# Optimization experiments

Hardware: AMD Instinct MI355X
Metric: run time of the kernel (lower is better)

The kernel has to match this reference:

```python
import jax, jax.numpy as jnp
import numpy as np

B, P, Q, N, D = 64, 12, 12, 1024, 64
DOW, TOD = 7, 288  # day-of-week / time-of-day one-hot depths (GMAN STEmbedding)


def setup_inputs() -> dict:
    key = jax.random.key(0)
    ks = iter(jax.random.split(key, 40))
    def g(shape, scale=0.05):
        return jax.random.normal(next(ks), shape, jnp.float32) * scale
    inp = {
        "X": jax.random.normal(next(ks), (B, P, N), jnp.float32),
        "ZC": jax.random.normal(next(ks), (B, P, 400), jnp.float32),
        "ZF": jax.random.normal(next(ks), (B, P, 1600), jnp.float32),
        "SE": g((N, D)),
        # STEmbedding FCs
        "W_se1": g((D, D)), "b_se1": jnp.zeros((D,), jnp.float32),
        "W_se2": g((D, D)), "b_se2": jnp.zeros((D,), jnp.float32),
        "W_te1": g((DOW + TOD, D)), "b_te1": jnp.zeros((D,), jnp.float32),
        "W_te2": g((D, D)), "b_te2": jnp.zeros((D,), jnp.float32),
        # FC_X_in
        "W_in1": g((1, D)), "b_in1": jnp.zeros((D,), jnp.float32),
        "W_in2": g((D, D)), "b_in2": jnp.zeros((D,), jnp.float32),
        # DCGRU layer 1 (gconv over [x||state, support@(x||state)] -> 4D input)
        "Wg1": g((4 * D, 2 * D)), "bg1": jnp.ones((2 * D,), jnp.float32),
        "Wc1": g((4 * D, D)), "bc1": jnp.zeros((D,), jnp.float32),
        # DCGRU layer 2
        "Wg2": g((4 * D, 2 * D)), "bg2": jnp.ones((2 * D,), jnp.float32),
        "Wc2": g((4 * D, D)), "bc2": jnp.zeros((D,), jnp.float32),
        # FC_X_out
        "W_o1": g((D, D)), "b_o1": jnp.zeros((D,), jnp.float32),
        "W_o2": g((D, Q)), "b_o2": jnp.zeros((Q,), jnp.float32),
        "TE": jax.random.randint(next(ks), (B, P + Q, 2), 0, 7, jnp.int32),
    }
    return inp


def _dcgru_scan(x_seq, support, Wg, bg, Wc, bc):
    """x_seq: [B,P,N,D] -> (sequence [B,P,N,D], last state [B,N,D])."""
    def gconv(x, s, W, b):
        z = jnp.concatenate([x, s], -1)                      # [B,N,2D]
        z1 = jnp.einsum('nm,bmd->bnd', support, z)           # diffusion step K=1
        return jnp.concatenate([z, z1], -1) @ W + b

    def step(state, x_t):
        ru = jax.nn.sigmoid(gconv(x_t, state, Wg, bg))       # [B,N,2D]
        r, u = jnp.split(ru, 2, axis=-1)
        c = jnp.tanh(gconv(x_t, r * state, Wc, bc))
        new = u * state + (1.0 - u) * c
        return new, new

    state0 = jnp.zeros(x_seq.shape[:1] + x_seq.shape[2:], x_seq.dtype)
    last, seq = jax.lax.scan(step, state0, jnp.swapaxes(x_seq, 0, 1))
    return jnp.swapaxes(seq, 0, 1), last


def reference(X, ZC, ZF, SE, W_se1, b_se1, W_se2, b_se2, W_te1, b_te1,
              W_te2, b_te2, W_in1, b_in1, W_in2, b_in2,
              Wg1, bg1, Wc1, bc1, Wg2, bg2, Wc2, bc2,
              W_o1, b_o1, W_o2, b_o2, TE):
    # adjacency is identity in this module; random_walk(I).T == I
    adj = jnp.eye(N, dtype=jnp.float32)
    support = (adj / jnp.sum(adj, axis=1, keepdims=True)).T

    # STEmbedding: spatial + temporal embedding
    se = jax.nn.relu(SE @ W_se1 + b_se1) @ W_se2 + b_se2                 # [N,D]
    te_oh = jnp.concatenate([
        jax.nn.one_hot(TE[..., 0], DOW, dtype=jnp.float32),
        jax.nn.one_hot(TE[..., 1], TOD, dtype=jnp.float32)], -1)        # [B,P+Q,295]
    te = jax.nn.relu(te_oh @ W_te1 + b_te1) @ W_te2 + b_te2              # [B,P+Q,D]
    STEX = (se[None, None] + te[:, :, None, :])[:, :P]                   # [B,P,N,D]

    # FC_X_in on expanded X, add STE
    Xe = X[..., None]                                                    # [B,P,N,1]
    Xe = jax.nn.relu(Xe @ W_in1 + b_in1) @ W_in2 + b_in2                 # [B,P,N,D]
    Xe = Xe + STEX

    seq1, _ = _dcgru_scan(Xe, support, Wg1, bg1, Wc1, bc1)               # [B,P,N,D]
    _, h = _dcgru_scan(seq1, support, Wg2, bg2, Wc2, bc2)                # [B,N,D]

    Y = jax.nn.relu(h @ W_o1 + b_o1) @ W_o2 + b_o2                       # [B,N,Q]
    return jnp.transpose(Y, (0, 2, 1))                                   # [B,Q,N]
```

## Files before the change

### kernel.cpp

```cpp
#include <hip/hip_runtime.h>


#define NB 1024

typedef float f32x4 __attribute__((ext_vector_type(4)));
typedef __bf16 bf16x8 __attribute__((ext_vector_type(8)));
typedef int i32x4 __attribute__((ext_vector_type(4)));

#define MFMA(a, b, c) __builtin_amdgcn_mfma_f32_16x16x32_bf16(a, b, c, 0, 0, 0)

__device__ __forceinline__ float fexp(float x) {
    return __builtin_amdgcn_exp2f(x * 1.44269504088896341f);
}
__device__ __forceinline__ float fsigmoid(float x) {
    return __builtin_amdgcn_rcpf(1.0f + fexp(-x));
}
__device__ __forceinline__ float ftanh(float x) {
    return 1.0f - 2.0f * __builtin_amdgcn_rcpf(1.0f + fexp(2.0f * x));
}

__device__ __forceinline__ bf16x8 ldfrag(const unsigned short* p) {
    i32x4 t = *(const i32x4*)p;
    return __builtin_bit_cast(bf16x8, t);
}
__device__ __forceinline__ void split8(f32x4 a0, f32x4 a1, bf16x8& hi, bf16x8& lo) {
    #pragma unroll
    for (int i = 0; i < 4; i++) {
        __bf16 h0 = (__bf16)a0[i]; hi[i] = h0;     lo[i] = (__bf16)(a0[i] - (float)h0);
        __bf16 h1 = (__bf16)a1[i]; hi[4 + i] = h1; lo[4 + i] = (__bf16)(a1[i] - (float)h1);
    }
}
__device__ __forceinline__ void wsplit(float v, unsigned short* dhi, unsigned short* dlo) {
    __bf16 h = (__bf16)v;
    __bf16 l = (__bf16)(v - (float)h);
    *dhi = __builtin_bit_cast(unsigned short, h);
    *dlo = __builtin_bit_cast(unsigned short, l);
}


__global__ void prep_gates(const float* __restrict__ Wg1, const float* __restrict__ Wg2,
                           unsigned short* __restrict__ fr) {
    int i = blockIdx.x * 256 + threadIdx.x;
    if (i >= 4096) return;
    int layer = i >> 11, r = i & 2047;
    int w = r >> 9; r &= 511; int nt = r >> 8; r &= 255; int ks = r >> 6; int lane = r & 63;
    const float* Wg = layer ? Wg2 : Wg1;
    int n = lane & 15, q = lane >> 4;
    int col = nt ? (64 + w * 16 + n) : (w * 16 + n);
    unsigned short* dst = fr + layer * 32768 + (((w * 2 + nt) * 4 + ks) * 2) * 512 + lane * 8;
    #pragma unroll
    for (int j = 0; j < 8; j++) {
        int k = ks * 32 + q * 8 + j;
        float v = Wg[k * 128 + col] + Wg[(k + 128) * 128 + col];
        wsplit(v, dst + j, dst + 512 + j);
    }
}

__global__ void prep_cand(const float* __restrict__ Wc1, const float* __restrict__ Wc2,
                          unsigned short* __restrict__ fr) {
    int i = blockIdx.x * 256 + threadIdx.x;
    if (i >= 2048) return;
    int layer = i >> 10, r = i & 1023;
    int w = r >> 8; r &= 255; int ks = r >> 6; int lane = r & 63;
    const float* Wc = layer ? Wc2 : Wc1;
    int n = lane & 15, q = lane >> 4;
    int col = w * 16 + n;
    unsigned short* dst = fr + 65536 + layer * 16384 + ((w * 4 + ks) * 2) * 512 + lane * 8;
    #pragma unroll
    for (int j = 0; j < 8; j++) {
        int k = ks * 32 + q * 8 + j;
        float v = Wc[k * 64 + col] + Wc[(k + 128) * 64 + col];
        wsplit(v, dst + j, dst + 512 + j);
    }
}

__global__ void prep_small(const float* __restrict__ Win2, const float* __restrict__ Wo1,
                           unsigned short* __restrict__ fr) {
    int i = blockIdx.x * 256 + threadIdx.x;
    if (i >= 1024) return;
    int kind = i >> 9, r = i & 511;
    int w = r >> 7; r &= 127; int ks = r >> 6; int lane = r & 63;
    const float* W = kind ? Wo1 : Win2;
    int n = lane & 15, q = lane >> 4;
    int col = w * 16 + n;
    unsigned short* dst = fr + 98304 + kind * 8192 + ((w * 2 + ks) * 2) * 512 + lane * 8;
    #pragma unroll
    for (int j = 0; j < 8; j++) {
        int k = ks * 32 + q * 8 + j;
        float v = W[k * 64 + col];
        wsplit(v, dst + j, dst + 512 + j);
    }
}

__global__ void prep_se(const float* __restrict__ SE, const float* __restrict__ W1,
                        const float* __restrict__ b1, const float* __restrict__ W2,
                        const float* __restrict__ b2, const float* __restrict__ bin2,
                        float* __restrict__ seB) {
    __shared__ float h[64];
    int n = blockIdx.x, d = threadIdx.x;
    float acc = b1[d];
    for (int k = 0; k < 64; k++) acc = fmaf(SE[n * 64 + k], W1[k * 64 + d], acc);
    h[d] = fmaxf(acc, 0.0f);
    __syncthreads();
    float acc2 = b2[d];
    for (int k = 0; k < 64; k++) acc2 = fmaf(h[k], W2[k * 64 + d], acc2);
    int nb = n >> 6, tok = n & 63;
    int mt = tok >> 4, q = (tok >> 2) & 3, r = tok & 3;
    int w = d >> 4, n16 = d & 15;
    seB[(((nb * 4 + w) * 64) + q * 16 + n16) * 16 + mt * 4 + r] = acc2 + bin2[d];
}

__global__ void prep_te(const int* __restrict__ TE, const float* __restrict__ W1,
                        const float* __restrict__ b1, const float* __restrict__ W2,
                        const float* __restrict__ b2, float* __restrict__ teo) {
    __shared__ float h[64];
    int bp = blockIdx.x;
    int b = bp / 12, p = bp - b * 12;
    int d = threadIdx.x;
    int dow = TE[(b * 24 + p) * 2 + 0];
    int tod = TE[(b * 24 + p) * 2 + 1];
    float v = W1[dow * 64 + d] + W1[(7 + tod) * 64 + d] + b1[d];
    h[d] = fmaxf(v, 0.0f);
    __syncthreads();
    float acc = b2[d];
    for (int k = 0; k < 64; k++) acc = fmaf(h[k], W2[k * 64 + d], acc);
    teo[bp * 64 + d] = acc;
}

#define SW(t, k) ((t) * 64 + ((k) ^ (((t) & 3) << 3) ^ ((t) & 4)))

__device__ __forceinline__ void lda_split(const float* __restrict__ src, int m, int k0,
                                          bf16x8& ahi, bf16x8& alo) {
    const int sk = (k0 ^ ((m & 3) << 3) ^ (m & 4));
    f32x4 a0 = *(const f32x4*)(src + m * 64 + sk);
    f32x4 a1 = *(const f32x4*)(src + m * 64 + (sk ^ 4));
    split8(a0, a1, ahi, alo);
}

__device__ __forceinline__ void gru_layer(
    const float* __restrict__ XIN, float* __restrict__ S, float* __restrict__ RS,
    const unsigned short* __restrict__ frG, const unsigned short* __restrict__ frC,
    const float* __restrict__ bg, const float* __restrict__ bc, int l, int w) {
    const int n16 = l & 15, q = l >> 4;
    const int col = w * 16 + n16;
    f32x4 accR[4], accU[4], accC[4];
    #pragma unroll
    for (int mt = 0; mt < 4; mt++) {
        accR[mt] = (f32x4)0.0f; accU[mt] = (f32x4)0.0f; accC[mt] = (f32x4)0.0f;
    }
    #pragma unroll
    for (int ks = 0; ks < 2; ks++) {
        bf16x8 bhiR = ldfrag(frG + ((0 * 4 + ks) * 2 + 0) * 512 + l * 8);
        bf16x8 bloR = ldfrag(frG + ((0 * 4 + ks) * 2 + 1) * 512 + l * 8);
        bf16x8 bhiU = ldfrag(frG + ((1 * 4 + ks) * 2 + 0) * 512 + l * 8);
        bf16x8 bloU = ldfrag(frG + ((1 * 4 + ks) * 2 + 1) * 512 + l * 8);
        bf16x8 bhiC = ldfrag(frC + (ks * 2 + 0) * 512 + l * 8);
        bf16x8 bloC = ldfrag(frC + (ks * 2 + 1) * 512 + l * 8);
        const int kk = ks * 32 + q * 8;
        #pragma unroll
        for (int mt = 0; mt < 4; mt++) {
            bf16x8 ahi, alo;
            lda_split(XIN, mt * 16 + n16, kk, ahi, alo);
            accR[mt] = MFMA(ahi, bhiR, accR[mt]);
            accR[mt] = MFMA(alo, bhiR, accR[mt]);
            accR[mt] = MFMA(ahi, bloR, accR[mt]);
            accU[mt] = MFMA(ahi, bhiU, accU[mt]);
            accU[mt] = MFMA(alo, bhiU, accU[mt]);
            accU[mt] = MFMA(ahi, bloU, accU[mt]);
            accC[mt] = MFMA(ahi, bhiC, accC[mt]);
            accC[mt] = MFMA(alo, bhiC, accC[mt]);
            accC[mt] = MFMA(ahi, bloC, accC[mt]);
        }
    }
    #pragma unroll
    for (int ks = 2; ks < 4; ks++) {
        bf16x8 bhiR = ldfrag(frG + ((0 * 4 + ks) * 2 + 0) * 512 + l * 8);
        bf16x8 bloR = ldfrag(frG + ((0 * 4 + ks) * 2 + 1) * 512 + l * 8);
        bf16x8 bhiU = ldfrag(frG + ((1 * 4 + ks) * 2 + 0) * 512 + l * 8);
        bf16x8 bloU = ldfrag(frG + ((1 * 4 + ks) * 2 + 1) * 512 + l * 8);
        const int kk = (ks - 2) * 32 + q * 8;
        #pragma unroll
        for (int mt = 0; mt < 4; mt++) {
            bf16x8 ahi, alo;
            lda_split(S, mt * 16 + n16, kk, ahi, alo);
            accR[mt] = MFMA(ahi, bhiR, accR[mt]);
            accR[mt] = MFMA(alo, bhiR, accR[mt]);
            accR[mt] = MFMA(ahi, bloR, accR[mt]);
            accU[mt] = MFMA(ahi, bhiU, accU[mt]);
            accU[mt] = MFMA(alo, bhiU, accU[mt]);
            accU[mt] = MFMA(ahi, bloU, accU[mt]);
        }
    }
    const float bgr = bg[col];
    #pragma unroll
    for (int mt = 0; mt < 4; mt++)
        #pragma unroll
        for (int r = 0; r < 4; r++) {
            int tok = mt * 16 + q * 4 + r;
            RS[SW(tok, col)] = fsigmoid(accR[mt][r] + bgr) * S[SW(tok, col)];
        }
    __syncthreads();
    #pragma unroll
    for (int ks = 2; ks < 4; ks++) {
        bf16x8 bhi = ldfrag(frC + (ks * 2 + 0) * 512 + l * 8);
        bf16x8 blo = ldfrag(frC + (ks * 2 + 1) * 512 + l * 8);
        const int kk = (ks - 2) * 32 + q * 8;
        #pragma unroll
        for (int mt = 0; mt < 4; mt++) {
            bf16x8 ahi, alo;
            lda_split(RS, mt * 16 + n16, kk, ahi, alo);
            accC[mt] = MFMA(ahi, bhi, accC[mt]);
            accC[mt] = MFMA(alo, bhi, accC[mt]);
            accC[mt] = MFMA(ahi, blo, accC[mt]);
        }
    }
    const float bcc = bc[col], bgu = bg[64 + col];
    #pragma unroll
    for (int mt = 0; mt < 4; mt++)
        #pragma unroll
        for (int r = 0; r < 4; r++) {
            int tok = mt * 16 + q * 4 + r;
            float u = fsigmoid(accU[mt][r] + bgu);
            float cnd = ftanh(accC[mt][r] + bcc);
            int a = SW(tok, col);
            S[a] = u * S[a] + (1.0f - u) * cnd;
        }
    __syncthreads();
}

__global__ __launch_bounds__(256, 2) void gman_main(
    const float* __restrict__ X, const float* __restrict__ ws,
    const float* __restrict__ Win1, const float* __restrict__ bin1,
    const float* __restrict__ bg1, const float* __restrict__ bc1,
    const float* __restrict__ bg2, const float* __restrict__ bc2,
    const float* __restrict__ bo1, const float* __restrict__ Wo2,
    const float* __restrict__ bo2, float* __restrict__ out) {
    __shared__ float XE[4096], S1[4096], S2[4096], RS[4096];

    const int tid = threadIdx.x;
    const int l = tid & 63;
    const int w = tid >> 6;
    const int n16 = l & 15, q = l >> 4;
    const int col = w * 16 + n16;
    const int b = blockIdx.x >> 4;
    const int nb = blockIdx.x & 15;
    const int n0 = nb << 6;

    const unsigned short* frU = (const unsigned short*)ws;
    const unsigned short* frG1 = frU + w * 8192;
    const unsigned short* frG2 = frU + 32768 + w * 8192;
    const unsigned short* frC1 = frU + 65536 + w * 4096;
    const unsigned short* frC2 = frU + 81920 + w * 4096;
    const unsigned short* frX  = frU + 98304 + w * 2048;
    const unsigned short* frH  = frU + 106496 + w * 2048;
    const float* seQ = ws + 57344 + (((nb * 4 + w) * 64) + l) * 16;
    const float* teo = ws + 122880;

    #pragma unroll
    for (int i = 0; i < 16; i++) { S1[tid + i * 256] = 0.0f; S2[tid + i * 256] = 0.0f; }

    f32x4 se[4];
    #pragma unroll
    for (int mt = 0; mt < 4; mt++) se[mt] = *(const f32x4*)(seQ + mt * 4);

    #pragma unroll 1
    for (int p = 0; p < 12; p++) {
        if (tid < 64) RS[tid] = X[(b * 12 + p) * NB + n0 + tid];
        __syncthreads();
        f32x4 accX[4];
        #pragma unroll
        for (int mt = 0; mt < 4; mt++) accX[mt] = (f32x4)0.0f;
        #pragma unroll
        for (int ks = 0; ks < 2; ks++) {
            const int k0 = ks * 32 + q * 8;
            f32x4 w1a = *(const f32x4*)(Win1 + k0), w1b = *(const f32x4*)(Win1 + k0 + 4);
            f32x4 b1a = *(const f32x4*)(bin1 + k0), b1b = *(const f32x4*)(bin1 + k0 + 4);
            bf16x8 bhi = ldfrag(frX + (ks * 2 + 0) * 512 + l * 8);
            bf16x8 blo = ldfrag(frX + (ks * 2 + 1) * 512 + l * 8);
            #pragma unroll
            for (int mt = 0; mt < 4; mt++) {
                const float xm = RS[mt * 16 + n16];
                f32x4 h0, h1v;
                #pragma unroll
                for (int i = 0; i < 4; i++) {
                    h0[i]  = fmaxf(fmaf(xm, w1a[i], b1a[i]), 0.0f);
                    h1v[i] = fmaxf(fmaf(xm, w1b[i], b1b[i]), 0.0f);
                }
                bf16x8 ahi, alo; split8(h0, h1v, ahi, alo);
                accX[mt] = MFMA(ahi, bhi, accX[mt]);
                accX[mt] = MFMA(alo, bhi, accX[mt]);
                accX[mt] = MFMA(ahi, blo, accX[mt]);
            }
        }
        const float tev = teo[(b * 12 + p) * 64 + col];
        __syncthreads();
        #pragma unroll
        for (int mt = 0; mt < 4; mt++)
            #pragma unroll
            for (int r = 0; r < 4; r++) {
                int tok = mt * 16 + q * 4 + r;
                XE[SW(tok, col)] = accX[mt][r] + se[mt][r] + tev;
            }
        __syncthreads();

        gru_layer(XE, S1, RS, frG1, frC1, bg1, bc1, l, w);
        gru_layer(S1, S2, RS, frG2, frC2, bg2, bc2, l, w);
    }

    f32x4 accH[4];
    #pragma unroll
    for (int mt = 0; mt < 4; mt++) accH[mt] = (f32x4)0.0f;
    #pragma unroll
    for (int ks = 0; ks < 2; ks++) {
        bf16x8 bhi = ldfrag(frH + (ks * 2 + 0) * 512 + l * 8);
        bf16x8 blo = ldfrag(frH + (ks * 2 + 1) * 512 + l * 8);
        const int kk = ks * 32 + q * 8;
        #pragma unroll
        for (int mt = 0; mt < 4; mt++) {
            bf16x8 ahi, alo;
            lda_split(S2, mt * 16 + n16, kk, ahi, alo);
            accH[mt] = MFMA(ahi, bhi, accH[mt]);
            accH[mt] = MFMA(alo, bhi, accH[mt]);
            accH[mt] = MFMA(ahi, blo, accH[mt]);
        }
    }
    const float bo = bo1[col];
    #pragma unroll
    for (int mt = 0; mt < 4; mt++)
        #pragma unroll
        for (int r = 0; r < 4; r++) {
            int tok = mt * 16 + q * 4 + r;
            XE[SW(tok, col)] = fmaxf(accH[mt][r] + bo, 0.0f);
        }
    __syncthreads();
    const int uw = __builtin_amdgcn_readfirstlane(w);
    float y0 = bo2[3 * uw], y1 = bo2[3 * uw + 1], y2 = bo2[3 * uw + 2];
    #pragma unroll 8
    for (int j = 0; j < 64; j++) {
        const float hj = XE[SW(l, j)];
        y0 = fmaf(hj, Wo2[j * 12 + 3 * uw + 0], y0);
        y1 = fmaf(hj, Wo2[j * 12 + 3 * uw + 1], y1);
        y2 = fmaf(hj, Wo2[j * 12 + 3 * uw + 2], y2);
    }
    out[(b * 12 + 3 * uw + 0) * NB + n0 + l] = y0;
    out[(b * 12 + 3 * uw + 1) * NB + n0 + l] = y1;
    out[(b * 12 + 3 * uw + 2) * NB + n0 + l] = y2;
}

extern "C" void kernel_launch(void* const* d_in, const int* in_sizes, int n_in,
                              void* d_out, int out_size, void* d_ws, size_t ws_size,
                              hipStream_t stream) {
    const float* X    = (const float*)d_in[0];
    const float* SE   = (const float*)d_in[3];
    const float* Wse1 = (const float*)d_in[4];
    const float* bse1 = (const float*)d_in[5];
    const float* Wse2 = (const float*)d_in[6];
    const float* bse2 = (const float*)d_in[7];
    const float* Wte1 = (const float*)d_in[8];
    const float* bte1 = (const float*)d_in[9];
    const float* Wte2 = (const float*)d_in[10];
    const float* bte2 = (const float*)d_in[11];
    const float* Win1 = (const float*)d_in[12];
    const float* bin1 = (const float*)d_in[13];
    const float* Win2 = (const float*)d_in[14];
    const float* bin2 = (const float*)d_in[15];
    const float* Wg1  = (const float*)d_in[16];
    const float* bg1  = (const float*)d_in[17];
    const float* Wc1  = (const float*)d_in[18];
    const float* bc1  = (const float*)d_in[19];
    const float* Wg2  = (const float*)d_in[20];
    const float* bg2  = (const float*)d_in[21];
    const float* Wc2  = (const float*)d_in[22];
    const float* bc2  = (const float*)d_in[23];
    const float* Wo1  = (const float*)d_in[24];
    const float* bo1  = (const float*)d_in[25];
    const float* Wo2  = (const float*)d_in[26];
    const float* bo2  = (const float*)d_in[27];
    const int*   TE   = (const int*)d_in[28];

    float* ws = (float*)d_ws;
    unsigned short* fr = (unsigned short*)ws;
    float* seB = ws + 57344;
    float* teo = ws + 122880;
    float* out = (float*)d_out;

    prep_gates<<<16, 256, 0, stream>>>(Wg1, Wg2, fr);
    prep_cand<<<8, 256, 0, stream>>>(Wc1, Wc2, fr);
    prep_small<<<4, 256, 0, stream>>>(Win2, Wo1, fr);
    prep_se<<<1024, 64, 0, stream>>>(SE, Wse1, bse1, Wse2, bse2, bin2, seB);
    prep_te<<<768, 64, 0, stream>>>(TE, Wte1, bte1, Wte2, bte2, teo);
    gman_main<<<1024, 256, 0, stream>>>(X, ws, Win1, bin1, bg1, bc1, bg2, bc2,
                                        bo1, Wo2, bo2, out);
}
```

Baseline: 580.2 us.

## Store activations as packed bf16 hi/lo pairs and double tokens per block

Shared-memory activations are now stored as packed 32-bit words holding the bf16 high and low parts, so MFMA operand loads become byte permutes instead of float-to-bf16 splitting on every read. Each block now covers 128 nodes with 512 threads (two halves of 4 waves), halving the block count. The input FC hidden layer is precomputed once into shared memory instead of being recomputed per wave, and bias/te loads are hoisted out of the time loop. Shared memory per block doubles to 128KB, which may limit occupancy. The packed split also differs slightly numerically, since the low part is truncated rather than rounded.

```diff
diff --git a/kernel.cpp b/kernel.cpp
--- a/kernel.cpp
+++ b/kernel.cpp
@@ -6,6 +6,7 @@
 typedef float f32x4 __attribute__((ext_vector_type(4)));
 typedef __bf16 bf16x8 __attribute__((ext_vector_type(8)));
 typedef int i32x4 __attribute__((ext_vector_type(4)));
+typedef unsigned int u32;
 
 #define MFMA(a, b, c) __builtin_amdgcn_mfma_f32_16x16x32_bf16(a, b, c, 0, 0, 0)
 
@@ -17,26 +18,52 @@
 }
 __device__ __forceinline__ float ftanh(float x) {
     return 1.0f - 2.0f * __builtin_amdgcn_rcpf(1.0f + fexp(2.0f * x));
+}
+
+__device__ __forceinline__ u32 packf(float v) {
+    u32 u = __builtin_bit_cast(u32, v);
+    u32 hb = u & 0xFFFF0000u;
+    float lo = v - __builtin_bit_cast(float, hb);
+    return hb | (__builtin_bit_cast(u32, lo) >> 16);
+}
+__device__ __forceinline__ float unpackf(u32 u) {
+    return __builtin_bit_cast(float, u & 0xFFFF0000u)
+         + __builtin_bit_cast(float, u << 16);
 }
 
 __device__ __forceinline__ bf16x8 ldfrag(const unsigned short* p) {
     i32x4 t = *(const i32x4*)p;
     return __builtin_bit_cast(bf16x8, t);
 }
-__device__ __forceinline__ void split8(f32x4 a0, f32x4 a1, bf16x8& hi, bf16x8& lo) {
-    #pragma unroll
-    for (int i = 0; i < 4; i++) {
-        __bf16 h0 = (__bf16)a0[i]; hi[i] = h0;     lo[i] = (__bf16)(a0[i] - (float)h0);
-        __bf16 h1 = (__bf16)a1[i]; hi[4 + i] = h1; lo[4 + i] = (__bf16)(a1[i] - (float)h1);
-    }
-}
+
+#define SWZ(t) (((((t) & 3) << 3)) ^ ((t) & 4) ^ (((t) & 8) << 1))
+#define SW(t, k) ((t) * 64 + ((k) ^ SWZ(t)))
+
+__device__ __forceinline__ void lda_packed(const u32* __restrict__ src, int m, int kk,
+                                           bf16x8& hi, bf16x8& lo) {
+    const int sk = kk ^ SWZ(m);
+    i32x4 d0 = *(const i32x4*)(src + m * 64 + sk);
+    i32x4 d1 = *(const i32x4*)(src + m * 64 + (sk ^ 4));
+    i32x4 h, L;
+    h[0] = (int)__builtin_amdgcn_perm((u32)d0[1], (u32)d0[0], 0x07060302u);
+    h[1] = (int)__builtin_amdgcn_perm((u32)d0[3], (u32)d0[2], 0x07060302u);
+    h[2] = (int)__builtin_amdgcn_perm((u32)d1[1], (u32)d1[0], 0x07060302u);
+    h[3] = (int)__builtin_amdgcn_perm((u32)d1[3], (u32)d1[2], 0x07060302u);
+    L[0] = (int)__builtin_amdgcn_perm((u32)d0[1], (u32)d0[0], 0x05040100u);
+    L[1] = (int)__builtin_amdgcn_perm((u32)d0[3], (u32)d0[2], 0x05040100u);
+    L[2] = (int)__builtin_amdgcn_perm((u32)d1[1], (u32)d1[0], 0x05040100u);
+    L[3] = (int)__builtin_amdgcn_perm((u32)d1[3], (u32)d1[2], 0x05040100u);
+    hi = __builtin_bit_cast(bf16x8, h);
+    lo = __builtin_bit_cast(bf16x8, L);
+}
+
+
 __device__ __forceinline__ void wsplit(float v, unsigned short* dhi, unsigned short* dlo) {
     __bf16 h = (__bf16)v;
     __bf16 l = (__bf16)(v - (float)h);
     *dhi = __builtin_bit_cast(unsigned short, h);
     *dlo = __builtin_bit_cast(unsigned short, l);
 }
-
 
 __global__ void prep_gates(const float* __restrict__ Wg1, const float* __restrict__ Wg2,
                            unsigned short* __restrict__ fr) {
@@ -104,10 +131,10 @@
     __syncthreads();
     float acc2 = b2[d];
     for (int k = 0; k < 64; k++) acc2 = fmaf(h[k], W2[k * 64 + d], acc2);
-    int nb = n >> 6, tok = n & 63;
-    int mt = tok >> 4, q = (tok >> 2) & 3, r = tok & 3;
-    int w = d >> 4, n16 = d & 15;
-    seB[(((nb * 4 + w) * 64) + q * 16 + n16) * 16 + mt * 4 + r] = acc2 + bin2[d];
+    int nb = n >> 7, mh = (n >> 6) & 1, mt = (n >> 4) & 3, qq = (n >> 2) & 3, r = n & 3;
+    int wq = d >> 4, n16 = d & 15;
+    int w8 = mh * 4 + wq, l = qq * 16 + n16;
+    seB[(((nb * 8 + w8) * 64) + l) * 16 + mt * 4 + r] = acc2 + bin2[d];
 }
 
 __global__ void prep_te(const int* __restrict__ TE, const float* __restrict__ W1,
@@ -127,22 +154,11 @@
     teo[bp * 64 + d] = acc;
 }
 
-#define SW(t, k) ((t) * 64 + ((k) ^ (((t) & 3) << 3) ^ ((t) & 4)))
-
-__device__ __forceinline__ void lda_split(const float* __restrict__ src, int m, int k0,
-                                          bf16x8& ahi, bf16x8& alo) {
-    const int sk = (k0 ^ ((m & 3) << 3) ^ (m & 4));
-    f32x4 a0 = *(const f32x4*)(src + m * 64 + sk);
-    f32x4 a1 = *(const f32x4*)(src + m * 64 + (sk ^ 4));
-    split8(a0, a1, ahi, alo);
-}
-
 __device__ __forceinline__ void gru_layer(
-    const float* __restrict__ XIN, float* __restrict__ S, float* __restrict__ RS,
+    const u32* __restrict__ XIN, u32* __restrict__ S, u32* __restrict__ RS,
     const unsigned short* __restrict__ frG, const unsigned short* __restrict__ frC,
-    const float* __restrict__ bg, const float* __restrict__ bc, int l, int w) {
+    float bgr, float bgu, float bcc, int l, int mh, int col) {
     const int n16 = l & 15, q = l >> 4;
-    const int col = w * 16 + n16;
     f32x4 accR[4], accU[4], accC[4];
     #pragma unroll
     for (int mt = 0; mt < 4; mt++) {
@@ -160,7 +176,7 @@
         #pragma unroll
         for (int mt = 0; mt < 4; mt++) {
             bf16x8 ahi, alo;
-            lda_split(XIN, mt * 16 + n16, kk, ahi, alo);
+            lda_packed(XIN, mh * 64 + mt * 16 + n16, kk, ahi, alo);
             accR[mt] = MFMA(ahi, bhiR, accR[mt]);
             accR[mt] = MFMA(alo, bhiR, accR[mt]);
             accR[mt] = MFMA(ahi, bloR, accR[mt]);
@@ -182,7 +198,7 @@
         #pragma unroll
         for (int mt = 0; mt < 4; mt++) {
             bf16x8 ahi, alo;
-            lda_split(S, mt * 16 + n16, kk, ahi, alo);
+            lda_packed(S, mh * 64 + mt * 16 + n16, kk, ahi, alo);
             accR[mt] = MFMA(ahi, bhiR, accR[mt]);
             accR[mt] = MFMA(alo, bhiR, accR[mt]);
             accR[mt] = MFMA(ahi, bloR, accR[mt]);
@@ -191,13 +207,13 @@
             accU[mt] = MFMA(ahi, bloU, accU[mt]);
         }
     }
-    const float bgr = bg[col];
     #pragma unroll
     for (int mt = 0; mt < 4; mt++)
         #pragma unroll
         for (int r = 0; r < 4; r++) {
-            int tok = mt * 16 + q * 4 + r;
-            RS[SW(tok, col)] = fsigmoid(accR[mt][r] + bgr) * S[SW(tok, col)];
+            int tok = mh * 64 + mt * 16 + q * 4 + r;
+            int a = SW(tok, col);
+            RS[a] = packf(fsigmoid(accR[mt][r] + bgr) * unpackf(S[a]));
         }
     __syncthreads();
     #pragma unroll
@@ -208,103 +224,120 @@
         #pragma unroll
         for (int mt = 0; mt < 4; mt++) {
             bf16x8 ahi, alo;
-            lda_split(RS, mt * 16 + n16, kk, ahi, alo);
+            lda_packed(RS, mh * 64 + mt * 16 + n16, kk, ahi, alo);
             accC[mt] = MFMA(ahi, bhi, accC[mt]);
             accC[mt] = MFMA(alo, bhi, accC[mt]);
             accC[mt] = MFMA(ahi, blo, accC[mt]);
         }
     }
-    const float bcc = bc[col], bgu = bg[64 + col];
     #pragma unroll
     for (int mt = 0; mt < 4; mt++)
         #pragma unroll
         for (int r = 0; r < 4; r++) {
-            int tok = mt * 16 + q * 4 + r;
+            int tok = mh * 64 + mt * 16 + q * 4 + r;
+            int a = SW(tok, col);
+            float sold = unpackf(S[a]);
             float u = fsigmoid(accU[mt][r] + bgu);
             float cnd = ftanh(accC[mt][r] + bcc);
-            int a = SW(tok, col);
-            S[a] = u * S[a] + (1.0f - u) * cnd;
+            S[a] = packf(u * sold + (1.0f - u) * cnd);
         }
     __syncthreads();
 }
 
-__global__ __launch_bounds__(256, 2) void gman_main(
+__global__ __launch_bounds__(512, 2) void gman_main(
     const float* __restrict__ X, const float* __restrict__ ws,
     const float* __restrict__ Win1, const float* __restrict__ bin1,
     const float* __restrict__ bg1, const float* __restrict__ bc1,
     const float* __restrict__ bg2, const float* __restrict__ bc2,
     const float* __restrict__ bo1, const float* __restrict__ Wo2,
     const float* __restrict__ bo2, float* __restrict__ out) {
-    __shared__ float XE[4096], S1[4096], S2[4096], RS[4096];
+    __shared__ u32 XE[8192], S1[8192], S2[8192], RS[8192];
 
     const int tid = threadIdx.x;
     const int l = tid & 63;
     const int w = tid >> 6;
+    const int uw = __builtin_amdgcn_readfirstlane(w);
+    const int uwq = uw & 3;
+    const int umh = uw >> 2;
     const int n16 = l & 15, q = l >> 4;
-    const int col = w * 16 + n16;
-    const int b = blockIdx.x >> 4;
-    const int nb = blockIdx.x & 15;
-    const int n0 = nb << 6;
+    const int col = uwq * 16 + n16;
+    const int b = blockIdx.x >> 3;
+    const int nb = blockIdx.x & 7;
+    const int n0 = nb << 7;
 
     const unsigned short* frU = (const unsigned short*)ws;
-    const unsigned short* frG1 = frU + w * 8192;
-    const unsigned short* frG2 = frU + 32768 + w * 8192;
-    const unsigned short* frC1 = frU + 65536 + w * 4096;
-    const unsigned short* frC2 = frU + 81920 + w * 4096;
-    const unsigned short* frX  = frU + 98304 + w * 2048;
-    const unsigned short* frH  = frU + 106496 + w * 2048;
-    const float* seQ = ws + 57344 + (((nb * 4 + w) * 64) + l) * 16;
+    const unsigned short* frG1 = frU + uwq * 8192;
+    const unsigned short* frG2 = frU + 32768 + uwq * 8192;
+    const unsigned short* frC1 = frU + 65536 + uwq * 4096;
+    const unsigned short* frC2 = frU + 81920 + uwq * 4096;
+    const unsigned short* frX  = frU + 98304 + uwq * 2048;
+    const unsigned short* frH  = frU + 106496 + uwq * 2048;
+    const float* seQ = ws + 57344 + (((nb * 8 + uw) * 64) + l) * 16;
     const float* teo = ws + 122880;
 
     #pragma unroll
-    for (int i = 0; i < 16; i++) { S1[tid + i * 256] = 0.0f; S2[tid + i * 256] = 0.0f; }
-
-    f32x4 se[4];
-    #pragma unroll
-    for (int mt = 0; mt < 4; mt++) se[mt] = *(const f32x4*)(seQ + mt * 4);
+    for (int i = 0; i < 16; i++) { S1[tid + i * 512] = 0u; S2[tid + i * 512] = 0u; }
+
+    f32x4 se_v[4];
+    #pragma unroll
+    for (int mt = 0; mt < 4; mt++) se_v[mt] = *(const f32x4*)(seQ + mt * 4);
+    float te_v[12];
+    #pragma unroll
+    for (int p = 0; p < 12; p++) te_v[p] = teo[(b * 12 + p) * 64 + col];
+    const float bg1r = bg1[col], bg1u = bg1[64 + col], bc1c = bc1[col];
+    const float bg2r = bg2[col], bg2u = bg2[64 + col], bc2c = bc2[col];
+    const float bo1c = bo1[col];
 
     #pragma unroll 1
     for (int p = 0; p < 12; p++) {
-        if (tid < 64) RS[tid] = X[(b * 12 + p) * NB + n0 + tid];
+        if (tid < 128) RS[tid] = __builtin_bit_cast(u32, X[(b * 12 + p) * NB + n0 + tid]);
+        __syncthreads();
+        const int t_h = tid >> 2, kc = tid & 3;
+        const float xv = __builtin_bit_cast(float, RS[t_h]);
+        u32 hp[16];
+        #pragma unroll
+        for (int i = 0; i < 16; i++) {
+            int k = kc * 16 + i;
+            hp[i] = packf(fmaxf(fmaf(xv, Win1[k], bin1[k]), 0.0f));
+        }
+        __syncthreads();
+        #pragma unroll
+        for (int c = 0; c < 4; c++) {
+            int z = (kc * 16 + c * 4) ^ SWZ(t_h);
+            i32x4 v;
+            v[0] = (int)hp[c * 4 + 0]; v[1] = (int)hp[c * 4 + 1];
+            v[2] = (int)hp[c * 4 + 2]; v[3] = (int)hp[c * 4 + 3];
+            *(i32x4*)(RS + t_h * 64 + z) = v;
+        }
         __syncthreads();
         f32x4 accX[4];
         #pragma unroll
         for (int mt = 0; mt < 4; mt++) accX[mt] = (f32x4)0.0f;
         #pragma unroll
         for (int ks = 0; ks < 2; ks++) {
-            const int k0 = ks * 32 + q * 8;
-            f32x4 w1a = *(const f32x4*)(Win1 + k0), w1b = *(const f32x4*)(Win1 + k0 + 4);
-            f32x4 b1a = *(const f32x4*)(bin1 + k0), b1b = *(const f32x4*)(bin1 + k0 + 4);
             bf16x8 bhi = ldfrag(frX + (ks * 2 + 0) * 512 + l * 8);
             bf16x8 blo = ldfrag(frX + (ks * 2 + 1) * 512 + l * 8);
+            const int kk = ks * 32 + q * 8;
             #pragma unroll
             for (int mt = 0; mt < 4; mt++) {
-                const float xm = RS[mt * 16 + n16];
-                f32x4 h0, h1v;
-                #pragma unroll
-                for (int i = 0; i < 4; i++) {
-                    h0[i]  = fmaxf(fmaf(xm, w1a[i], b1a[i]), 0.0f);
-                    h1v[i] = fmaxf(fmaf(xm, w1b[i], b1b[i]), 0.0f);
-                }
-                bf16x8 ahi, alo; split8(h0, h1v, ahi, alo);
+                bf16x8 ahi, alo;
+                lda_packed(RS, umh * 64 + mt * 16 + n16, kk, ahi, alo);
                 accX[mt] = MFMA(ahi, bhi, accX[mt]);
                 accX[mt] = MFMA(alo, bhi, accX[mt]);
                 accX[mt] = MFMA(ahi, blo, accX[mt]);
             }
         }
-        const float tev = teo[(b * 12 + p) * 64 + col];
-        __syncthreads();
         #pragma unroll
         for (int mt = 0; mt < 4; mt++)
             #pragma unroll
             for (int r = 0; r < 4; r++) {
-                int tok = mt * 16 + q * 4 + r;
-                XE[SW(tok, col)] = accX[mt][r] + se[mt][r] + tev;
+                int tok = umh * 64 + mt * 16 + q * 4 + r;
+                XE[SW(tok, col)] = packf(accX[mt][r] + se_v[mt][r] + te_v[p]);
             }
         __syncthreads();
 
-        gru_layer(XE, S1, RS, frG1, frC1, bg1, bc1, l, w);
-        gru_layer(S1, S2, RS, frG2, frC2, bg2, bc2, l, w);
+        gru_layer(XE, S1, RS, frG1, frC1, bg1r, bg1u, bc1c, l, umh, col);
+        gru_layer(S1, S2, RS, frG2, frC2, bg2r, bg2u, bc2c, l, umh, col);
     }
 
     f32x4 accH[4];
@@ -318,33 +351,40 @@
         #pragma unroll
         for (int mt = 0; mt < 4; mt++) {
             bf16x8 ahi, alo;
-            lda_split(S2, mt * 16 + n16, kk, ahi, alo);
+            lda_packed(S2, umh * 64 + mt * 16 + n16, kk, ahi, alo);
             accH[mt] = MFMA(ahi, bhi, accH[mt]);
             accH[mt] = MFMA(alo, bhi, accH[mt]);
             accH[mt] = MFMA(ahi, blo, accH[mt]);
         }
     }
-    const float bo = bo1[col];
     #pragma unroll
     for (int mt = 0; mt < 4; mt++)
         #pragma unroll
         for (int r = 0; r < 4; r++) {
-            int tok = mt * 16 + q * 4 + r;
-            XE[SW(tok, col)] = fmaxf(accH[mt][r] + bo, 0.0f);
+            int tok = umh * 64 + mt * 16 + q * 4 + r;
+            XE[SW(tok, col)] = packf(fmaxf(accH[mt][r] + bo1c, 0.0f));
         }
     __syncthreads();
-    const int uw = __builtin_amdgcn_readfirstlane(w);
-    float y0 = bo2[3 * uw], y1 = bo2[3 * uw + 1], y2 = bo2[3 * uw + 2];
-    #pragma unroll 8
-    for (int j = 0; j < 64; j++) {
-        const float hj = XE[SW(l, j)];
-        y0 = fmaf(hj, Wo2[j * 12 + 3 * uw + 0], y0);
-        y1 = fmaf(hj, Wo2[j * 12 + 3 * uw + 1], y1);
-        y2 = fmaf(hj, Wo2[j * 12 + 3 * uw + 2], y2);
-    }
-    out[(b * 12 + 3 * uw + 0) * NB + n0 + l] = y0;
-    out[(b * 12 + 3 * uw + 1) * NB + n0 + l] = y1;
-    out[(b * 12 + 3 * uw + 2) * NB + n0 + l] = y2;
+    const int tt = tid & 127;
+    const int ug = uw >> 1;
+    const int swzt = SWZ(tt);
+    float y0 = bo2[3 * ug + 0], y1 = bo2[3 * ug + 1], y2 = bo2[3 * ug + 2];
+    #pragma unroll
+    for (int c = 0; c < 16; c++) {
+        i32x4 d = *(const i32x4*)(XE + tt * 64 + c * 4);
+        const int j0 = (c * 4) ^ swzt;
+        #pragma unroll
+        for (int e = 0; e < 4; e++) {
+            float hj = unpackf((u32)d[e]);
+            int j = j0 + e;
+            y0 = fmaf(hj, Wo2[j * 12 + 3 * ug + 0], y0);
+            y1 = fmaf(hj, Wo2[j * 12 + 3 * ug + 1], y1);
+            y2 = fmaf(hj, Wo2[j * 12 + 3 * ug + 2], y2);
+        }
+    }
+    out[(b * 12 + 3 * ug + 0) * NB + n0 + tt] = y0;
+    out[(b * 12 + 3 * ug + 1) * NB + n0 + tt] = y1;
+    out[(b * 12 + 3 * ug + 2) * NB + n0 + tt] = y2;
 }
 
 extern "C" void kernel_launch(void* const* d_in, const int* in_sizes, int n_in,
@@ -389,6 +429,6 @@
     prep_small<<<4, 256, 0, stream>>>(Win2, Wo1, fr);
     prep_se<<<1024, 64, 0, stream>>>(SE, Wse1, bse1, Wse2, bse2, bin2, seB);
     prep_te<<<768, 64, 0, stream>>>(TE, Wte1, bte1, Wte2, bte2, teo);
-    gman_main<<<1024, 256, 0, stream>>>(X, ws, Win1, bin1, bg1, bc1, bg2, bc2,
-                                        bo1, Wo2, bo2, out);
-}
+    gman_main<<<512, 512, 0, stream>>>(X, ws, Win1, bin1, bg1, bc1, bg2, bc2,
+                                       bo1, Wo2, bo2, out);
+}
```

Result: slower. 643.6 us (+10.9%).

## Store LDS activations as packed bf16 hi/lo pairs and keep gate weights in registers

Applied to the files above, without the earlier changes.

Activations in shared memory are now stored as a packed u32 holding the bf16 high part and a bf16 residual. A-fragments are therefore built with v_perm byte shuffles instead of a float-to-bf16 split on every load. The gate weight fragments for both GRU layers are loaded once into registers before the time loop rather than reloaded from global memory each step, and biases are hoisted. The swizzle gains an extra bit, the output projection reads LDS with vector loads, and the old gru_layer is left behind as a dead stub. The register-resident gate fragments add 64 VGPRs per layer pair, which risks spills or lower occupancy under the 256x2 launch bound.

```diff
diff --git a/kernel.cpp b/kernel.cpp
--- a/kernel.cpp
+++ b/kernel.cpp
@@ -6,6 +6,7 @@
 typedef float f32x4 __attribute__((ext_vector_type(4)));
 typedef __bf16 bf16x8 __attribute__((ext_vector_type(8)));
 typedef int i32x4 __attribute__((ext_vector_type(4)));
+typedef unsigned int u32;
 
 #define MFMA(a, b, c) __builtin_amdgcn_mfma_f32_16x16x32_bf16(a, b, c, 0, 0, 0)
 
@@ -17,6 +18,17 @@
 }
 __device__ __forceinline__ float ftanh(float x) {
     return 1.0f - 2.0f * __builtin_amdgcn_rcpf(1.0f + fexp(2.0f * x));
+}
+
+__device__ __forceinline__ u32 packf(float v) {
+    u32 u = __builtin_bit_cast(u32, v);
+    u32 hb = u & 0xFFFF0000u;
+    float lo = v - __builtin_bit_cast(float, hb);
+    return hb | (__builtin_bit_cast(u32, lo) >> 16);
+}
+__device__ __forceinline__ float unpackf(u32 u) {
+    return __builtin_bit_cast(float, u & 0xFFFF0000u)
+         + __builtin_bit_cast(float, u << 16);
 }
 
 __device__ __forceinline__ bf16x8 ldfrag(const unsigned short* p) {
@@ -30,13 +42,35 @@
         __bf16 h1 = (__bf16)a1[i]; hi[4 + i] = h1; lo[4 + i] = (__bf16)(a1[i] - (float)h1);
     }
 }
+
+#define SWZ(t) ((((t) & 3) << 3) ^ ((t) & 4) ^ (((t) & 8) << 1))
+#define SW(t, k) ((t) * 64 + ((k) ^ SWZ(t)))
+
+__device__ __forceinline__ void lda_packed(const u32* __restrict__ src, int m, int kk,
+                                           bf16x8& hi, bf16x8& lo) {
+    const int sk = kk ^ SWZ(m);
+    i32x4 d0 = *(const i32x4*)(src + m * 64 + sk);
+    i32x4 d1 = *(const i32x4*)(src + m * 64 + (sk ^ 4));
+    i32x4 h, L;
+    h[0] = (int)__builtin_amdgcn_perm((u32)d0[1], (u32)d0[0], 0x07060302u);
+    h[1] = (int)__builtin_amdgcn_perm((u32)d0[3], (u32)d0[2], 0x07060302u);
+    h[2] = (int)__builtin_amdgcn_perm((u32)d1[1], (u32)d1[0], 0x07060302u);
+    h[3] = (int)__builtin_amdgcn_perm((u32)d1[3], (u32)d1[2], 0x07060302u);
+    L[0] = (int)__builtin_amdgcn_perm((u32)d0[1], (u32)d0[0], 0x05040100u);
+    L[1] = (int)__builtin_amdgcn_perm((u32)d0[3], (u32)d0[2], 0x05040100u);
+    L[2] = (int)__builtin_amdgcn_perm((u32)d1[1], (u32)d1[0], 0x05040100u);
+    L[3] = (int)__builtin_amdgcn_perm((u32)d1[3], (u32)d1[2], 0x05040100u);
+    hi = __builtin_bit_cast(bf16x8, h);
+    lo = __builtin_bit_cast(bf16x8, L);
+}
+
+
 __device__ __forceinline__ void wsplit(float v, unsigned short* dhi, unsigned short* dlo) {
     __bf16 h = (__bf16)v;
     __bf16 l = (__bf16)(v - (float)h);
     *dhi = __builtin_bit_cast(unsigned short, h);
     *dlo = __builtin_bit_cast(unsigned short, l);
 }
-
 
 __global__ void prep_gates(const float* __restrict__ Wg1, const float* __restrict__ Wg2,
                            unsigned short* __restrict__ fr) {
@@ -127,22 +161,11 @@
     teo[bp * 64 + d] = acc;
 }
 
-#define SW(t, k) ((t) * 64 + ((k) ^ (((t) & 3) << 3) ^ ((t) & 4)))
-
-__device__ __forceinline__ void lda_split(const float* __restrict__ src, int m, int k0,
-                                          bf16x8& ahi, bf16x8& alo) {
-    const int sk = (k0 ^ ((m & 3) << 3) ^ (m & 4));
-    f32x4 a0 = *(const f32x4*)(src + m * 64 + sk);
-    f32x4 a1 = *(const f32x4*)(src + m * 64 + (sk ^ 4));
-    split8(a0, a1, ahi, alo);
-}
-
 __device__ __forceinline__ void gru_layer(
-    const float* __restrict__ XIN, float* __restrict__ S, float* __restrict__ RS,
-    const unsigned short* __restrict__ frG, const unsigned short* __restrict__ frC,
-    const float* __restrict__ bg, const float* __restrict__ bc, int l, int w) {
+    const u32* __restrict__ XIN, u32* __restrict__ S, u32* __restrict__ RS,
+    const bf16x8 (&g)[16], const unsigned short* __restrict__ frC,
+    float bgr, float bgu, float bcc, int l) {
     const int n16 = l & 15, q = l >> 4;
-    const int col = w * 16 + n16;
     f32x4 accR[4], accU[4], accC[4];
     #pragma unroll
     for (int mt = 0; mt < 4; mt++) {
@@ -150,23 +173,19 @@
     }
     #pragma unroll
     for (int ks = 0; ks < 2; ks++) {
-        bf16x8 bhiR = ldfrag(frG + ((0 * 4 + ks) * 2 + 0) * 512 + l * 8);
-        bf16x8 bloR = ldfrag(frG + ((0 * 4 + ks) * 2 + 1) * 512 + l * 8);
-        bf16x8 bhiU = ldfrag(frG + ((1 * 4 + ks) * 2 + 0) * 512 + l * 8);
-        bf16x8 bloU = ldfrag(frG + ((1 * 4 + ks) * 2 + 1) * 512 + l * 8);
         bf16x8 bhiC = ldfrag(frC + (ks * 2 + 0) * 512 + l * 8);
         bf16x8 bloC = ldfrag(frC + (ks * 2 + 1) * 512 + l * 8);
         const int kk = ks * 32 + q * 8;
         #pragma unroll
         for (int mt = 0; mt < 4; mt++) {
             bf16x8 ahi, alo;
-            lda_split(XIN, mt * 16 + n16, kk, ahi, alo);
-            accR[mt] = MFMA(ahi, bhiR, accR[mt]);
-            accR[mt] = MFMA(alo, bhiR, accR[mt]);
-            accR[mt] = MFMA(ahi, bloR, accR[mt]);
-            accU[mt] = MFMA(ahi, bhiU, accU[mt]);
-            accU[mt] = MFMA(alo, bhiU, accU[mt]);
-            accU[mt] = MFMA(ahi, bloU, accU[mt]);
+            lda_packed(XIN, mt * 16 + n16, kk, ahi, alo);
+            accR[mt] = MFMA(ahi, g[(0 * 4 + ks) * 2 + 0], accR[mt]);
+            accR[mt] = MFMA(alo, g[(0 * 4 + ks) * 2 + 0], accR[mt]);
+            accR[mt] = MFMA(ahi, g[(0 * 4 + ks) * 2 + 1], accR[mt]);
+            accU[mt] = MFMA(ahi, g[(1 * 4 + ks) * 2 + 0], accU[mt]);
+            accU[mt] = MFMA(alo, g[(1 * 4 + ks) * 2 + 0], accU[mt]);
+            accU[mt] = MFMA(ahi, g[(1 * 4 + ks) * 2 + 1], accU[mt]);
             accC[mt] = MFMA(ahi, bhiC, accC[mt]);
             accC[mt] = MFMA(alo, bhiC, accC[mt]);
             accC[mt] = MFMA(ahi, bloC, accC[mt]);
@@ -174,30 +193,76 @@
     }
     #pragma unroll
     for (int ks = 2; ks < 4; ks++) {
-        bf16x8 bhiR = ldfrag(frG + ((0 * 4 + ks) * 2 + 0) * 512 + l * 8);
-        bf16x8 bloR = ldfrag(frG + ((0 * 4 + ks) * 2 + 1) * 512 + l * 8);
-        bf16x8 bhiU = ldfrag(frG + ((1 * 4 + ks) * 2 + 0) * 512 + l * 8);
-        bf16x8 bloU = ldfrag(frG + ((1 * 4 + ks) * 2 + 1) * 512 + l * 8);
         const int kk = (ks - 2) * 32 + q * 8;
         #pragma unroll
         for (int mt = 0; mt < 4; mt++) {
             bf16x8 ahi, alo;
-            lda_split(S, mt * 16 + n16, kk, ahi, alo);
-            accR[mt] = MFMA(ahi, bhiR, accR[mt]);
-            accR[mt] = MFMA(alo, bhiR, accR[mt]);
-            accR[mt] = MFMA(ahi, bloR, accR[mt]);
-            accU[mt] = MFMA(ahi, bhiU, accU[mt]);
-            accU[mt] = MFMA(alo, bhiU, accU[mt]);
-            accU[mt] = MFMA(ahi, bloU, accU[mt]);
-        }
-    }
-    const float bgr = bg[col];
+            lda_packed(S, mt * 16 + n16, kk, ahi, alo);
+            accR[mt] = MFMA(ahi, g[(0 * 4 + ks) * 2 + 0], accR[mt]);
+            accR[mt] = MFMA(alo, g[(0 * 4 + ks) * 2 + 0], accR[mt]);
+            accR[mt] = MFMA(ahi, g[(0 * 4 + ks) * 2 + 1], accR[mt]);
+            accU[mt] = MFMA(ahi, g[(1 * 4 + ks) * 2 + 0], accU[mt]);
+            accU[mt] = MFMA(alo, g[(1 * 4 + ks) * 2 + 0], accU[mt]);
+            accU[mt] = MFMA(ahi, g[(1 * 4 + ks) * 2 + 1], accU[mt]);
+        }
+    }
+    const int col = (l & 15) + ((l >> 4) & 0);
+    (void)col;
+    (void)bgr; (void)bgu; (void)bcc; (void)RS;
+}
+
+__device__ __forceinline__ void gru_full(
+    const u32* __restrict__ XIN, u32* __restrict__ S, u32* __restrict__ RS,
+    const bf16x8 (&g)[16], const unsigned short* __restrict__ frC,
+    float bgr, float bgu, float bcc, int l, int col) {
+    const int n16 = l & 15, q = l >> 4;
+    f32x4 accR[4], accU[4], accC[4];
+    #pragma unroll
+    for (int mt = 0; mt < 4; mt++) {
+        accR[mt] = (f32x4)0.0f; accU[mt] = (f32x4)0.0f; accC[mt] = (f32x4)0.0f;
+    }
+    #pragma unroll
+    for (int ks = 0; ks < 2; ks++) {
+        bf16x8 bhiC = ldfrag(frC + (ks * 2 + 0) * 512 + l * 8);
+        bf16x8 bloC = ldfrag(frC + (ks * 2 + 1) * 512 + l * 8);
+        const int kk = ks * 32 + q * 8;
+        #pragma unroll
+        for (int mt = 0; mt < 4; mt++) {
+            bf16x8 ahi, alo;
+            lda_packed(XIN, mt * 16 + n16, kk, ahi, alo);
+            accR[mt] = MFMA(ahi, g[ks * 2 + 0], accR[mt]);
+            accR[mt] = MFMA(alo, g[ks * 2 + 0], accR[mt]);
+            accR[mt] = MFMA(ahi, g[ks * 2 + 1], accR[mt]);
+            accU[mt] = MFMA(ahi, g[8 + ks * 2 + 0], accU[mt]);
+            accU[mt] = MFMA(alo, g[8 + ks * 2 + 0], accU[mt]);
+            accU[mt] = MFMA(ahi, g[8 + ks * 2 + 1], accU[mt]);
+            accC[mt] = MFMA(ahi, bhiC, accC[mt]);
+            accC[mt] = MFMA(alo, bhiC, accC[mt]);
+            accC[mt] = MFMA(ahi, bloC, accC[mt]);
+        }
+    }
+    #pragma unroll
+    for (int ks = 2; ks < 4; ks++) {
+        const int kk = (ks - 2) * 32 + q * 8;
+        #pragma unroll
+        for (int mt = 0; mt < 4; mt++) {
+            bf16x8 ahi, alo;
+            lda_packed(S, mt * 16 + n16, kk, ahi, alo);
+            accR[mt] = MFMA(ahi, g[ks * 2 + 0], accR[mt]);
+            accR[mt] = MFMA(alo, g[ks * 2 + 0], accR[mt]);
+            accR[mt] = MFMA(ahi, g[ks * 2 + 1], accR[mt]);
+            accU[mt] = MFMA(ahi, g[8 + ks * 2 + 0], accU[mt]);
+            accU[mt] = MFMA(alo, g[8 + ks * 2 + 0], accU[mt]);
+            accU[mt] = MFMA(ahi, g[8 + ks * 2 + 1], accU[mt]);
+        }
+    }
     #pragma unroll
     for (int mt = 0; mt < 4; mt++)
         #pragma unroll
         for (int r = 0; r < 4; r++) {
             int tok = mt * 16 + q * 4 + r;
-            RS[SW(tok, col)] = fsigmoid(accR[mt][r] + bgr) * S[SW(tok, col)];
+            int a = SW(tok, col);
+            RS[a] = packf(fsigmoid(accR[mt][r] + bgr) * unpackf(S[a]));
         }
     __syncthreads();
     #pragma unroll
@@ -208,22 +273,22 @@
         #pragma unroll
         for (int mt = 0; mt < 4; mt++) {
             bf16x8 ahi, alo;
-            lda_split(RS, mt * 16 + n16, kk, ahi, alo);
+            lda_packed(RS, mt * 16 + n16, kk, ahi, alo);
             accC[mt] = MFMA(ahi, bhi, accC[mt]);
             accC[mt] = MFMA(alo, bhi, accC[mt]);
             accC[mt] = MFMA(ahi, blo, accC[mt]);
         }
     }
-    const float bcc = bc[col], bgu = bg[64 + col];
     #pragma unroll
     for (int mt = 0; mt < 4; mt++)
         #pragma unroll
         for (int r = 0; r < 4; r++) {
             int tok = mt * 16 + q * 4 + r;
+            int a = SW(tok, col);
+            float sold = unpackf(S[a]);
             float u = fsigmoid(accU[mt][r] + bgu);
             float cnd = ftanh(accC[mt][r] + bcc);
-            int a = SW(tok, col);
-            S[a] = u * S[a] + (1.0f - u) * cnd;
+            S[a] = packf(u * sold + (1.0f - u) * cnd);
         }
     __syncthreads();
 }
@@ -235,37 +300,46 @@
     const float* __restrict__ bg2, const float* __restrict__ bc2,
     const float* __restrict__ bo1, const float* __restrict__ Wo2,
     const float* __restrict__ bo2, float* __restrict__ out) {
-    __shared__ float XE[4096], S1[4096], S2[4096], RS[4096];
+    __shared__ u32 XE[4096], S1[4096], S2[4096], RS[4096];
 
     const int tid = threadIdx.x;
     const int l = tid & 63;
     const int w = tid >> 6;
+    const int uw = __builtin_amdgcn_readfirstlane(w);
     const int n16 = l & 15, q = l >> 4;
-    const int col = w * 16 + n16;
+    const int col = uw * 16 + n16;
     const int b = blockIdx.x >> 4;
     const int nb = blockIdx.x & 15;
     const int n0 = nb << 6;
 
     const unsigned short* frU = (const unsigned short*)ws;
-    const unsigned short* frG1 = frU + w * 8192;
-    const unsigned short* frG2 = frU + 32768 + w * 8192;
-    const unsigned short* frC1 = frU + 65536 + w * 4096;
-    const unsigned short* frC2 = frU + 81920 + w * 4096;
-    const unsigned short* frX  = frU + 98304 + w * 2048;
-    const unsigned short* frH  = frU + 106496 + w * 2048;
-    const float* seQ = ws + 57344 + (((nb * 4 + w) * 64) + l) * 16;
+    const unsigned short* frG1 = frU + uw * 8192;
+    const unsigned short* frG2 = frU + 32768 + uw * 8192;
+    const unsigned short* frC1 = frU + 65536 + uw * 4096;
+    const unsigned short* frC2 = frU + 81920 + uw * 4096;
+    const unsigned short* frX  = frU + 98304 + uw * 2048;
+    const unsigned short* frH  = frU + 106496 + uw * 2048;
+    const float* seQ = ws + 57344 + (((nb * 4 + uw) * 64) + l) * 16;
     const float* teo = ws + 122880;
 
     #pragma unroll
-    for (int i = 0; i < 16; i++) { S1[tid + i * 256] = 0.0f; S2[tid + i * 256] = 0.0f; }
-
-    f32x4 se[4];
-    #pragma unroll
-    for (int mt = 0; mt < 4; mt++) se[mt] = *(const f32x4*)(seQ + mt * 4);
+    for (int i = 0; i < 16; i++) { S1[tid + i * 256] = 0u; S2[tid + i * 256] = 0u; }
+
+    bf16x8 g1[16], g2[16];
+    #pragma unroll
+    for (int i = 0; i < 16; i++) g1[i] = ldfrag(frG1 + i * 512 + l * 8);
+    #pragma unroll
+    for (int i = 0; i < 16; i++) g2[i] = ldfrag(frG2 + i * 512 + l * 8);
+
+    f32x4 se_v[4];
+    #pragma unroll
+    for (int mt = 0; mt < 4; mt++) se_v[mt] = *(const f32x4*)(seQ + mt * 4);
+    const float bg1r = bg1[col], bg1u = bg1[64 + col], bc1c = bc1[col];
+    const float bg2r = bg2[col], bg2u = bg2[64 + col], bc2c = bc2[col];
 
     #pragma unroll 1
     for (int p = 0; p < 12; p++) {
-        if (tid < 64) RS[tid] = X[(b * 12 + p) * NB + n0 + tid];
+        if (tid < 64) RS[tid] = __builtin_bit_cast(u32, X[(b * 12 + p) * NB + n0 + tid]);
         __syncthreads();
         f32x4 accX[4];
         #pragma unroll
@@ -279,7 +353,7 @@
             bf16x8 blo = ldfrag(frX + (ks * 2 + 1) * 512 + l * 8);
             #pragma unroll
             for (int mt = 0; mt < 4; mt++) {
-                const float xm = RS[mt * 16 + n16];
+                const float xm = __builtin_bit_cast(float, RS[mt * 16 + n16]);
                 f32x4 h0, h1v;
                 #pragma unroll
                 for (int i = 0; i < 4; i++) {
@@ -299,12 +373,12 @@
             #pragma unroll
             for (int r = 0; r < 4; r++) {
                 int tok = mt * 16 + q * 4 + r;
-                XE[SW(tok, col)] = accX[mt][r] + se[mt][r] + tev;
+                XE[SW(tok, col)] = packf(accX[mt][r] + se_v[mt][r] + tev);
             }
         __syncthreads();
 
-        gru_layer(XE, S1, RS, frG1, frC1, bg1, bc1, l, w);
-        gru_layer(S1, S2, RS, frG2, frC2, bg2, bc2, l, w);
+        gru_full(XE, S1, RS, g1, frC1, bg1r, bg1u, bc1c, l, col);
+        gru_full(S1, S2, RS, g2, frC2, bg2r, bg2u, bc2c, l, col);
     }
 
     f32x4 accH[4];
@@ -318,29 +392,35 @@
         #pragma unroll
         for (int mt = 0; mt < 4; mt++) {
             bf16x8 ahi, alo;
-            lda_split(S2, mt * 16 + n16, kk, ahi, alo);
+            lda_packed(S2, mt * 16 + n16, kk, ahi, alo);
             accH[mt] = MFMA(ahi, bhi, accH[mt]);
             accH[mt] = MFMA(alo, bhi, accH[mt]);
             accH[mt] = MFMA(ahi, blo, accH[mt]);
         }
     }
-    const float bo = bo1[col];
+    const float bo1c = bo1[col];
     #pragma unroll
     for (int mt = 0; mt < 4; mt++)
         #pragma unroll
         for (int r = 0; r < 4; r++) {
             int tok = mt * 16 + q * 4 + r;
-            XE[SW(tok, col)] = fmaxf(accH[mt][r] + bo, 0.0f);
+            XE[SW(tok, col)] = packf(fmaxf(accH[mt][r] + bo1c, 0.0f));
         }
     __syncthreads();
-    const int uw = __builtin_amdgcn_readfirstlane(w);
-    float y0 = bo2[3 * uw], y1 = bo2[3 * uw + 1], y2 = bo2[3 * uw + 2];
-    #pragma unroll 8
-    for (int j = 0; j < 64; j++) {
-        const float hj = XE[SW(l, j)];
-        y0 = fmaf(hj, Wo2[j * 12 + 3 * uw + 0], y0);
-        y1 = fmaf(hj, Wo2[j * 12 + 3 * uw + 1], y1);
-        y2 = fmaf(hj, Wo2[j * 12 + 3 * uw + 2], y2);
+    const int swzt = SWZ(l);
+    float y0 = bo2[3 * uw + 0], y1 = bo2[3 * uw + 1], y2 = bo2[3 * uw + 2];
+    #pragma unroll
+    for (int c = 0; c < 16; c++) {
+        i32x4 d = *(const i32x4*)(XE + l * 64 + c * 4);
+        const int j0 = (c * 4) ^ swzt;
+        #pragma unroll
+        for (int e = 0; e < 4; e++) {
+            float hj = unpackf((u32)d[e]);
+            int j = j0 + e;
+            y0 = fmaf(hj, Wo2[j * 12 + 3 * uw + 0], y0);
+            y1 = fmaf(hj, Wo2[j * 12 + 3 * uw + 1], y1);
+            y2 = fmaf(hj, Wo2[j * 12 + 3 * uw + 2], y2);
+        }
     }
     out[(b * 12 + 3 * uw + 0) * NB + n0 + l] = y0;
     out[(b * 12 + 3 * uw + 1) * NB + n0 + l] = y1;
```

Result: no change. 583.4 us (+0.5%).
